# Kernel tuning notes

Hardware: AMD Instinct MI355X
Metric: run time of the kernel (lower is better)

The kernel has to match this reference:

```python
import jax, jax.numpy as jnp
import numpy as np
from jax import lax

B, T, D_MODEL = 4, 2048, 2048
EXPAND, D_CONV = 2, 4
D_INNER = D_MODEL * EXPAND


def setup_inputs() -> dict:
    key = jax.random.key(0)
    ks = jax.random.split(key, 5)
    x = jax.random.normal(ks[0], (B, T, D_MODEL), dtype=jnp.float32)
    w_in = jax.random.normal(ks[1], (2 * D_INNER, D_MODEL), dtype=jnp.float32) * (D_MODEL ** -0.5)
    w_out = jax.random.normal(ks[2], (D_MODEL, D_INNER), dtype=jnp.float32) * (D_INNER ** -0.5)
    conv_w = jax.random.normal(ks[3], (D_INNER, 1, D_CONV), dtype=jnp.float32) * (D_CONV ** -0.5)
    conv_b = jax.random.normal(ks[4], (D_INNER,), dtype=jnp.float32) * 0.02
    D = jnp.ones((D_INNER,), dtype=jnp.float32)
    return {"x": x, "w_in": w_in, "w_out": w_out, "conv_w": conv_w, "conv_b": conv_b, "D": D}


def _forward(x, w_in, w_out, conv_w, conv_b, D):
    # in_proj: [B,T,C] @ [C, 2*d_inner]
    x_proj = jnp.einsum('btc,dc->btd', x, w_in)
    xi, gate = jnp.split(x_proj, 2, axis=-1)  # each [B,T,d_inner]
    # depthwise causal conv1d: torch pads both sides by d_conv-1 then truncates
    # output to first T positions -> equivalent to left-pad (d_conv-1), valid conv.
    xc = jnp.transpose(xi, (0, 2, 1))  # [B, d_inner, T]
    xc = lax.conv_general_dilated(
        xc, conv_w,
        window_strides=(1,),
        padding=[(D_CONV - 1, 0)],
        dimension_numbers=('NCH', 'OIH', 'NCH'),
        feature_group_count=D_INNER,
    ) + conv_b[None, :, None]
    xc = jnp.transpose(xc, (0, 2, 1))  # [B, T, d_inner]
    h = jax.nn.silu(xc) * D[None, None, :] * jax.nn.silu(gate)
    return jnp.einsum('btd,cd->btc', h, w_out)


def reference(x, w_in, w_out, conv_w, conv_b, D):
    return _forward(x, w_in, w_out, conv_w, conv_b, D)
```

## Files before the change

### kernel.cpp

```cpp
#include <hip/hip_runtime.h>
#include <hip/hip_bf16.h>
#include <stdint.h>
#include <string.h>


#define BT_TOTAL 8192
#define DM 2048
#define DI 4096

typedef __attribute__((ext_vector_type(8)))  short short8;
typedef __attribute__((ext_vector_type(16))) float f32x16;

__device__ __forceinline__ void async_ld16(const void* g, void* l) {
    __builtin_amdgcn_global_load_lds(
        (__attribute__((address_space(1))) void*)g,
        (__attribute__((address_space(3))) void*)l,
        16, 0, 0);
}

__device__ __forceinline__ float bf2f(ushort u) {
    union { uint i; float f; } v; v.i = ((uint)u) << 16; return v.f;
}

__device__ __forceinline__ ushort f2bf_bits(float f) {
    union { __hip_bfloat16 b; ushort u; } v;
    v.b = __float2bfloat16(f);
    return v.u;
}

template<bool OUT_BF16>
__global__ __launch_bounds__(256) void gemm_bt_kernel(
    const ushort* __restrict__ A, const ushort* __restrict__ B,
    void* __restrict__ Cp, int M, int N, int K)
{
    __shared__ ushort As[128 * 64];
    __shared__ ushort Bs[128 * 64];

    const int tid  = threadIdx.x;
    const int lane = tid & 63;
    const int wave = tid >> 6;
    const int wm   = (wave >> 1) * 64;
    const int wn   = (wave & 1) * 64;
    const int l31  = lane & 31;
    const int half = lane >> 5;

    const int bm = blockIdx.y * 128;
    const int bn = blockIdx.x * 128;

    f32x16 acc[2][2];
#pragma unroll
    for (int i = 0; i < 2; ++i)
#pragma unroll
        for (int j = 0; j < 2; ++j)
#pragma unroll
            for (int r = 0; r < 16; ++r)
                acc[i][j][r] = 0.f;

    int aoff[4], boff[4];
    ushort* al[4];
    ushort* bl[4];
#pragma unroll
    for (int t = 0; t < 4; ++t) {
        const int c  = tid + t * 256;
        const int r  = c >> 3;
        const int fr = (r ^ (r >> 3)) & 7;
        const int co = ((c & 7) ^ fr) * 8;
        aoff[t] = (bm + r) * K + co;
        boff[t] = (bn + r) * K + co;
        al[t] = &As[c * 8];
        bl[t] = &Bs[c * 8];
    }

    const ushort* aP[8];
    const ushort* bP[8];
#pragma unroll
    for (int s = 0; s < 4; ++s)
#pragma unroll
        for (int tt = 0; tt < 2; ++tt) {
            const int rowA = wm + tt * 32 + l31;
            const int rowB = wn + tt * 32 + l31;
            const int fA = (rowA ^ (rowA >> 3)) & 7;
            const int fB = (rowB ^ (rowB >> 3)) & 7;
            const int q = s * 2 + half;
            aP[s * 2 + tt] = &As[rowA * 64 + (q ^ fA) * 8];
            bP[s * 2 + tt] = &Bs[rowB * 64 + (q ^ fB) * 8];
        }

    for (int kk = 0; kk < K; kk += 64) {
        const ushort* Ak = A + kk;
        const ushort* Bk = B + kk;
        __syncthreads();
#pragma unroll
        for (int t = 0; t < 4; ++t) {
            async_ld16(Ak + aoff[t], al[t]);
            async_ld16(Bk + boff[t], bl[t]);
        }
        __syncthreads();

#pragma unroll
        for (int s = 0; s < 4; ++s) {
            short8 af[2], bf[2];
#pragma unroll
            for (int tt = 0; tt < 2; ++tt) {
                af[tt] = *(const short8*)aP[s * 2 + tt];
                bf[tt] = *(const short8*)bP[s * 2 + tt];
            }
#pragma unroll
            for (int tm = 0; tm < 2; ++tm)
#pragma unroll
                for (int tn = 0; tn < 2; ++tn)
                    acc[tm][tn] = __builtin_amdgcn_mfma_f32_32x32x16_bf16(
                        af[tm], bf[tn], acc[tm][tn], 0, 0, 0);
        }
    }

    const int col0  = bn + wn + l31;
    const int rbase = bm + wm + 4 * half;
    if (OUT_BF16) {
        __hip_bfloat16* C = (__hip_bfloat16*)Cp;
#pragma unroll
        for (int tm = 0; tm < 2; ++tm)
#pragma unroll
            for (int tn = 0; tn < 2; ++tn)
#pragma unroll
                for (int r = 0; r < 16; ++r) {
                    const int row = rbase + tm * 32 + (r & 3) + 8 * (r >> 2);
                    C[(size_t)row * (size_t)N + col0 + tn * 32] =
                        __float2bfloat16(acc[tm][tn][r]);
                }
    } else {
        float* C = (float*)Cp;
#pragma unroll
        for (int tm = 0; tm < 2; ++tm)
#pragma unroll
            for (int tn = 0; tn < 2; ++tn)
#pragma unroll
                for (int r = 0; r < 16; ++r) {
                    const int row = rbase + tm * 32 + (r & 3) + 8 * (r >> 2);
                    C[(size_t)row * (size_t)N + col0 + tn * 32] = acc[tm][tn][r];
                }
    }
}

__global__ __launch_bounds__(256) void conv_silu_kernel(
    const ushort* __restrict__ xp,
    const float* __restrict__ cw,
    const float* __restrict__ cb,
    const float* __restrict__ Dv,
    ushort* __restrict__ h)
{
    const int v  = blockIdx.x * 256 + threadIdx.x;
    const int d8 = (v & 511) * 8;
    const int bt = v >> 9;
    const int t  = bt & 2047;

    const uint4 gv = *(const uint4*)(xp + (size_t)bt * (2 * DI) + DI + d8);
    uint4 tap[4];
#pragma unroll
    for (int k = 0; k < 4; ++k) {
        const int tt = t - 3 + k;
        if (tt >= 0)
            tap[k] = *(const uint4*)(xp + (size_t)(bt - 3 + k) * (2 * DI) + d8);
        else
            tap[k] = (uint4){0u, 0u, 0u, 0u};
    }

    const float4* cwv = (const float4*)(cw + (size_t)d8 * 4);
    const float4  cb0 = *(const float4*)(cb + d8);
    const float4  cb1 = *(const float4*)(cb + d8 + 4);
    const float4  dv0 = *(const float4*)(Dv + d8);
    const float4  dv1 = *(const float4*)(Dv + d8 + 4);
    const float cbs[8] = {cb0.x, cb0.y, cb0.z, cb0.w, cb1.x, cb1.y, cb1.z, cb1.w};
    const float dvs[8] = {dv0.x, dv0.y, dv0.z, dv0.w, dv1.x, dv1.y, dv1.z, dv1.w};

    ushort res[8];
#pragma unroll
    for (int j = 0; j < 8; ++j) {
        float a = cbs[j];
        const float4 w = cwv[j];
        const float wk[4] = {w.x, w.y, w.z, w.w};
#pragma unroll
        for (int k = 0; k < 4; ++k) {
            const uint u = ((const uint*)&tap[k])[j >> 1];
            const ushort us = (j & 1) ? (ushort)(u >> 16) : (ushort)(u & 0xffff);
            a += bf2f(us) * wk[k];
        }
        const uint gu = ((const uint*)&gv)[j >> 1];
        const ushort gs = (j & 1) ? (ushort)(gu >> 16) : (ushort)(gu & 0xffff);
        const float g = bf2f(gs);
        const float sc = a / (1.f + __expf(-a));
        const float sg = g / (1.f + __expf(-g));
        res[j] = f2bf_bits(sc * dvs[j] * sg);
    }
    *(uint4*)(h + (size_t)bt * DI + d8) = *(const uint4*)res;
}

__global__ __launch_bounds__(256) void f32_to_bf16_x4(
    const float* __restrict__ in, __hip_bfloat16* __restrict__ out, int n4)
{
    const int i = blockIdx.x * 256 + threadIdx.x;
    if (i >= n4) return;
    const float4 v = *(const float4*)(in + (size_t)i * 4);
    union { __hip_bfloat16 hh[4]; ushort4 u; } cv;
    cv.hh[0] = __float2bfloat16(v.x);
    cv.hh[1] = __float2bfloat16(v.y);
    cv.hh[2] = __float2bfloat16(v.z);
    cv.hh[3] = __float2bfloat16(v.w);
    *(ushort4*)((ushort*)out + (size_t)i * 4) = cv.u;
}

extern "C" void kernel_launch(void* const* d_in, const int* in_sizes, int n_in,
                              void* d_out, int out_size, void* d_ws, size_t ws_size,
                              hipStream_t stream)
{
    const float* x     = (const float*)d_in[0];
    const float* w_in  = (const float*)d_in[1];
    const float* w_out = (const float*)d_in[2];
    const float* cw    = (const float*)d_in[3];
    const float* cb    = (const float*)d_in[4];
    const float* Dv    = (const float*)d_in[5];
    float* out = (float*)d_out;

    char* wsc = (char*)d_ws;
    __hip_bfloat16* xproj = (__hip_bfloat16*)wsc;
    __hip_bfloat16* xb    = (__hip_bfloat16*)(wsc + (size_t)134217728);
    __hip_bfloat16* winb  = (__hip_bfloat16*)(wsc + (size_t)134217728 + 33554432);
    __hip_bfloat16* hbuf  = (__hip_bfloat16*)(wsc + (size_t)134217728);
    __hip_bfloat16* woutb = (__hip_bfloat16*)(wsc + (size_t)201326592);

    f32_to_bf16_x4<<<(BT_TOTAL * DM / 4 + 255) / 256, 256, 0, stream>>>(x, xb, BT_TOTAL * DM / 4);
    f32_to_bf16_x4<<<(2 * DI * DM / 4 + 255) / 256, 256, 0, stream>>>(w_in, winb, 2 * DI * DM / 4);
    f32_to_bf16_x4<<<(DM * DI / 4 + 255) / 256, 256, 0, stream>>>(w_out, woutb, DM * DI / 4);

    gemm_bt_kernel<true><<<dim3(2 * DI / 128, BT_TOTAL / 128), 256, 0, stream>>>(
        (const ushort*)xb, (const ushort*)winb, xproj, BT_TOTAL, 2 * DI, DM);

    conv_silu_kernel<<<(BT_TOTAL * DI / 8) / 256, 256, 0, stream>>>(
        (const ushort*)xproj, cw, cb, Dv, (ushort*)hbuf);

    gemm_bt_kernel<false><<<dim3(DM / 128, BT_TOTAL / 128), 256, 0, stream>>>(
        (const ushort*)hbuf, (const ushort*)woutb, out, BT_TOTAL, DM, DI);
}
```

Baseline: 715.7 us.

## Rewrite GEMM as 256x256 tile, 8-wave double-buffered pipelined kernel with XCD remap

The GEMM moves from 128x128 tiles with 4 waves and a single LDS buffer to 256x256 tiles with 8 waves and double-buffered LDS. Global-to-LDS async loads for the next K chunks are interleaved with MFMA phases, using hand-placed barriers, vmcnt/lgkmcnt waits and s_setprio. A workgroup index remap spreads neighbouring tiles across XCDs. The aim is to hide memory latency and raise arithmetic intensity, at the cost of fragile hand synchronisation and 128 KB of LDS per block.

```diff
diff --git a/kernel.cpp b/kernel.cpp
--- a/kernel.cpp
+++ b/kernel.cpp
@@ -28,116 +28,182 @@
     return v.u;
 }
 
+#define RA0 0
+#define RB0 16384
+#define RA1 32768
+#define RB1 49152
+
+#define BAR()   asm volatile("s_barrier" ::: "memory")
+#define LGKM0() asm volatile("s_waitcnt lgkmcnt(0)" ::: "memory")
+#define VM6()   asm volatile("s_waitcnt vmcnt(6)" ::: "memory")
+#define VM0()   asm volatile("s_waitcnt vmcnt(0)" ::: "memory")
+#define PRIO1() __builtin_amdgcn_s_setprio(1)
+#define PRIO0() __builtin_amdgcn_s_setprio(0)
+
 template<bool OUT_BF16>
-__global__ __launch_bounds__(256) void gemm_bt_kernel(
+__global__ __launch_bounds__(512, 2) void gemm256_kernel(
     const ushort* __restrict__ A, const ushort* __restrict__ B,
     void* __restrict__ Cp, int M, int N, int K)
 {
-    __shared__ ushort As[128 * 64];
-    __shared__ ushort Bs[128 * 64];
+    __shared__ ushort lds[65536];
 
     const int tid  = threadIdx.x;
     const int lane = tid & 63;
     const int wave = tid >> 6;
-    const int wm   = (wave >> 1) * 64;
-    const int wn   = (wave & 1) * 64;
+    const int wm   = wave >> 2;
+    const int wn   = wave & 3;
     const int l31  = lane & 31;
     const int half = lane >> 5;
 
-    const int bm = blockIdx.y * 128;
-    const int bn = blockIdx.x * 128;
-
-    f32x16 acc[2][2];
-#pragma unroll
-    for (int i = 0; i < 2; ++i)
-#pragma unroll
-        for (int j = 0; j < 2; ++j)
+    const int nbx = gridDim.x;
+    const int nwg = nbx * gridDim.y;
+    int orig = blockIdx.y * nbx + blockIdx.x;
+    orig = (orig & 7) * (nwg >> 3) + (orig >> 3);
+    const int bn = (orig % nbx) * 256;
+    const int bm = (orig / nbx) * 256;
+
+    const int rq = tid >> 3;
+    const int jq = tid & 7;
+    const int fq = (rq ^ (rq >> 3)) & 7;
+    const int goffA = (bm + rq) * K + ((jq ^ fq) * 8);
+    const int goffB = (bn + rq) * K + ((jq ^ fq) * 8);
+    const int dst8  = tid * 8;
+
+    const int flane = (l31 ^ (l31 >> 3)) & 7;
+    const int cl8   = (half ^ flane) * 8;
+    const int aBase = (wm * 128 + l31) * 64;
+    const int bBase = (wn * 64  + l31) * 64;
+
+    f32x16 acc[4][2];
+#pragma unroll
+    for (int m = 0; m < 4; ++m)
+#pragma unroll
+        for (int n = 0; n < 2; ++n)
 #pragma unroll
             for (int r = 0; r < 16; ++r)
-                acc[i][j][r] = 0.f;
-
-    int aoff[4], boff[4];
-    ushort* al[4];
-    ushort* bl[4];
-#pragma unroll
-    for (int t = 0; t < 4; ++t) {
-        const int c  = tid + t * 256;
-        const int r  = c >> 3;
-        const int fr = (r ^ (r >> 3)) & 7;
-        const int co = ((c & 7) ^ fr) * 8;
-        aoff[t] = (bm + r) * K + co;
-        boff[t] = (bn + r) * K + co;
-        al[t] = &As[c * 8];
-        bl[t] = &Bs[c * 8];
-    }
-
-    const ushort* aP[8];
-    const ushort* bP[8];
-#pragma unroll
-    for (int s = 0; s < 4; ++s)
-#pragma unroll
-        for (int tt = 0; tt < 2; ++tt) {
-            const int rowA = wm + tt * 32 + l31;
-            const int rowB = wn + tt * 32 + l31;
-            const int fA = (rowA ^ (rowA >> 3)) & 7;
-            const int fB = (rowB ^ (rowB >> 3)) & 7;
-            const int q = s * 2 + half;
-            aP[s * 2 + tt] = &As[rowA * 64 + (q ^ fA) * 8];
-            bP[s * 2 + tt] = &Bs[rowB * 64 + (q ^ fB) * 8];
-        }
-
-    for (int kk = 0; kk < K; kk += 64) {
-        const ushort* Ak = A + kk;
-        const ushort* Bk = B + kk;
-        __syncthreads();
-#pragma unroll
-        for (int t = 0; t < 4; ++t) {
-            async_ld16(Ak + aoff[t], al[t]);
-            async_ld16(Bk + boff[t], bl[t]);
-        }
-        __syncthreads();
-
-#pragma unroll
-        for (int s = 0; s < 4; ++s) {
-            short8 af[2], bf[2];
-#pragma unroll
-            for (int tt = 0; tt < 2; ++tt) {
-                af[tt] = *(const short8*)aP[s * 2 + tt];
-                bf[tt] = *(const short8*)bP[s * 2 + tt];
-            }
-#pragma unroll
-            for (int tm = 0; tm < 2; ++tm)
-#pragma unroll
-                for (int tn = 0; tn < 2; ++tn)
-                    acc[tm][tn] = __builtin_amdgcn_mfma_f32_32x32x16_bf16(
-                        af[tm], bf[tn], acc[tm][tn], 0, 0, 0);
-        }
-    }
-
-    const int col0  = bn + wn + l31;
-    const int rbase = bm + wm + 4 * half;
+                acc[m][n][r] = 0.f;
+
+    short8 aE[4], aO[4], b0[4], b1[4];
+
+#define STA(P, QROW, REG) async_ld16((P) + (size_t)(QROW) * K + goffA, \
+                                     &lds[(REG) + (QROW) * 64 + dst8])
+#define STB(P, QROW, REG) async_ld16((P) + (size_t)(QROW) * K + goffB, \
+                                     &lds[(REG) + (QROW) * 64 + dst8])
+
+#define RDA(MH, REG) do { \
+    _Pragma("unroll") \
+    for (int ks = 0; ks < 4; ++ks) { \
+        aE[ks] = *(const short8*)&lds[(REG) + aBase + (MH)*4096 + (cl8 ^ (ks<<4))]; \
+        aO[ks] = *(const short8*)&lds[(REG) + aBase + (MH)*4096 + 2048 + (cl8 ^ (ks<<4) ^ 32)]; \
+    } } while (0)
+
+#define RDB(DSTV, NF, REG) do { \
+    _Pragma("unroll") \
+    for (int ks = 0; ks < 4; ++ks) { \
+        DSTV[ks] = *(const short8*)&lds[(REG) + bBase + (NF)*2048 + (cl8 ^ (ks<<4) ^ ((NF)<<5))]; \
+    } } while (0)
+
+#define MMA(MH, NH, BF) do { \
+    _Pragma("unroll") \
+    for (int ks = 0; ks < 4; ++ks) { \
+        acc[(MH)*2    ][(NH)] = __builtin_amdgcn_mfma_f32_32x32x16_bf16( \
+            aE[ks], BF[ks], acc[(MH)*2    ][(NH)], 0, 0, 0); \
+        acc[(MH)*2 + 1][(NH)] = __builtin_amdgcn_mfma_f32_32x32x16_bf16( \
+            aO[ks], BF[ks], acc[(MH)*2 + 1][(NH)], 0, 0, 0); \
+    } } while (0)
+
+    {
+        STA(A, 0, RA0);  STA(A, 128, RA0);
+        STB(B, 0, RB0);  STB(B, 128, RB0);
+        STA(A, 64, RA0); STA(A, 192, RA0);
+        STB(B, 64, RB0); STB(B, 192, RB0);
+        const ushort* Ap = A + 64;
+        const ushort* Bp = B + 64;
+        STA(Ap, 0, RA1);  STA(Ap, 128, RA1);
+        STB(Bp, 0, RB1);  STB(Bp, 128, RB1);
+        STA(Ap, 64, RA1); STA(Ap, 192, RA1);
+        VM6(); BAR();
+    }
+
+    const int NITER = K >> 7;
+    for (int i = 0; i < NITER; ++i) {
+        const bool last = (i == NITER - 1);
+        const int k1 = 128 * i + 64;
+        const int k2 = 128 * i + 128;
+        const int k3 = 128 * i + 192;
+
+        RDA(0, RA0); RDB(b0, 0, RB0);
+        STB(B + k1, 64, RB1); STB(B + k1, 192, RB1);
+        BAR(); LGKM0();
+        PRIO1(); MMA(0, 0, b0); PRIO0();
+        BAR();
+
+        RDB(b1, 1, RB0);
+        if (!last) { STA(A + k2, 0, RA0); STA(A + k2, 128, RA0); }
+        BAR(); LGKM0();
+        PRIO1(); MMA(0, 1, b1); PRIO0();
+        BAR();
+
+        RDA(1, RA0);
+        if (!last) { STB(B + k2, 0, RB0); STB(B + k2, 128, RB0); }
+        BAR(); LGKM0();
+        PRIO1(); MMA(1, 1, b1); PRIO0();
+        BAR();
+
+        if (!last) { STA(A + k2, 64, RA0); STA(A + k2, 192, RA0); }
+        BAR();
+        PRIO1(); MMA(1, 0, b0); PRIO0();
+        if (last) { VM0(); } else { VM6(); }
+        BAR();
+
+        RDA(0, RA1); RDB(b0, 0, RB1);
+        if (!last) { STB(B + k2, 64, RB0); STB(B + k2, 192, RB0); }
+        BAR(); LGKM0();
+        PRIO1(); MMA(0, 0, b0); PRIO0();
+        BAR();
+
+        RDB(b1, 1, RB1);
+        if (!last) { STA(A + k3, 0, RA1); STA(A + k3, 128, RA1); }
+        BAR(); LGKM0();
+        PRIO1(); MMA(0, 1, b1); PRIO0();
+        BAR();
+
+        RDA(1, RA1);
+        if (!last) { STB(B + k3, 0, RB1); STB(B + k3, 128, RB1); }
+        BAR(); LGKM0();
+        PRIO1(); MMA(1, 1, b1); PRIO0();
+        BAR();
+
+        if (!last) { STA(A + k3, 64, RA1); STA(A + k3, 192, RA1); }
+        BAR();
+        PRIO1(); MMA(1, 0, b0); PRIO0();
+        if (!last) { VM6(); BAR(); }
+    }
+
+    const int col0 = bn + wn * 64 + l31;
+    const int row0 = bm + wm * 128 + 4 * half;
     if (OUT_BF16) {
         __hip_bfloat16* C = (__hip_bfloat16*)Cp;
 #pragma unroll
-        for (int tm = 0; tm < 2; ++tm)
-#pragma unroll
-            for (int tn = 0; tn < 2; ++tn)
+        for (int m = 0; m < 4; ++m)
+#pragma unroll
+            for (int n = 0; n < 2; ++n)
 #pragma unroll
                 for (int r = 0; r < 16; ++r) {
-                    const int row = rbase + tm * 32 + (r & 3) + 8 * (r >> 2);
-                    C[(size_t)row * (size_t)N + col0 + tn * 32] =
-                        __float2bfloat16(acc[tm][tn][r]);
+                    const int row = row0 + m * 32 + (r & 3) + 8 * (r >> 2);
+                    C[(size_t)row * (size_t)N + col0 + n * 32] =
+                        __float2bfloat16(acc[m][n][r]);
                 }
     } else {
         float* C = (float*)Cp;
 #pragma unroll
-        for (int tm = 0; tm < 2; ++tm)
-#pragma unroll
-            for (int tn = 0; tn < 2; ++tn)
+        for (int m = 0; m < 4; ++m)
+#pragma unroll
+            for (int n = 0; n < 2; ++n)
 #pragma unroll
                 for (int r = 0; r < 16; ++r) {
-                    const int row = rbase + tm * 32 + (r & 3) + 8 * (r >> 2);
-                    C[(size_t)row * (size_t)N + col0 + tn * 32] = acc[tm][tn][r];
+                    const int row = row0 + m * 32 + (r & 3) + 8 * (r >> 2);
+                    C[(size_t)row * (size_t)N + col0 + n * 32] = acc[m][n][r];
                 }
     }
 }
@@ -232,12 +298,12 @@
     f32_to_bf16_x4<<<(2 * DI * DM / 4 + 255) / 256, 256, 0, stream>>>(w_in, winb, 2 * DI * DM / 4);
     f32_to_bf16_x4<<<(DM * DI / 4 + 255) / 256, 256, 0, stream>>>(w_out, woutb, DM * DI / 4);
 
-    gemm_bt_kernel<true><<<dim3(2 * DI / 128, BT_TOTAL / 128), 256, 0, stream>>>(
+    gemm256_kernel<true><<<dim3((2 * DI) / 256, BT_TOTAL / 256), 512, 0, stream>>>(
         (const ushort*)xb, (const ushort*)winb, xproj, BT_TOTAL, 2 * DI, DM);
 
     conv_silu_kernel<<<(BT_TOTAL * DI / 8) / 256, 256, 0, stream>>>(
         (const ushort*)xproj, cw, cb, Dv, (ushort*)hbuf);
 
-    gemm_bt_kernel<false><<<dim3(DM / 128, BT_TOTAL / 128), 256, 0, stream>>>(
+    gemm256_kernel<false><<<dim3(DM / 256, BT_TOTAL / 256), 512, 0, stream>>>(
         (const ushort*)hbuf, (const ushort*)woutb, out, BT_TOTAL, DM, DI);
 }
```

Result: faster. 646.5 us (-9.7%).
